# Optimization experiments

Hardware: AMD Instinct MI355X
Metric: run time of the kernel (lower is better)

## Reference

```python
import jax, jax.numpy as jnp
import numpy as np
from jax import lax

NUM_CLASSES = 10
NUM_ITER = 3
CAP_DIM = 8       # primary capsule dim
OUT_CAP_DIM = 16  # digit capsule dim
NUM_MAP = 32      # 256 / 8
NUM_PRIM = 144    # 12*12


def squash(x, axis=-1):
    s2 = jnp.sum(x * x, axis=axis, keepdims=True)
    return (s2 / (1.0 + s2)) * x / jnp.sqrt(s2 + 1e-8)


def conv2d(x, w, b):
    y = lax.conv_general_dilated(x, w, (1, 1), 'VALID',
                                 dimension_numbers=('NCHW', 'OIHW', 'NCHW'))
    return y + b[None, :, None, None]


def setup_inputs() -> dict:
    key = jax.random.key(0)
    ks = jax.random.split(key, 13)
    B = 128
    return {
        'imgs': jax.random.uniform(ks[0], (B, 1, 28, 28), dtype=jnp.float32),
        'conv1_w': jax.random.normal(ks[1], (256, 1, 9, 9), jnp.float32) * 0.05,
        'conv1_b': jnp.zeros((256,), jnp.float32),
        'conv2_w': jax.random.normal(ks[2], (256, 256, 9, 9), jnp.float32) * 0.02,
        'conv2_b': jnp.zeros((256,), jnp.float32),
        # non-shared routing weights: [num_prim_map, num_prim_cap, num_classes, out_dim, in_dim]
        'W_digit': jax.random.normal(ks[3], (NUM_MAP, NUM_PRIM, NUM_CLASSES, OUT_CAP_DIM, CAP_DIM), jnp.float32),
        'dec_w1': jax.random.normal(ks[4], (OUT_CAP_DIM * NUM_CLASSES, 512), jnp.float32) * 0.05,
        'dec_b1': jnp.zeros((512,), jnp.float32),
        'dec_w2': jax.random.normal(ks[5], (512, 1024), jnp.float32) * 0.04,
        'dec_b2': jnp.zeros((1024,), jnp.float32),
        'dec_w3': jax.random.normal(ks[6], (1024, 784), jnp.float32) * 0.03,
        'dec_b3': jnp.zeros((784,), jnp.float32),
    }


def capsnet_fwd(imgs, conv1_w, conv1_b, conv2_w, conv2_b, W_digit,
                dec_w1, dec_b1, dec_w2, dec_b2, dec_w3, dec_b3):
    B = imgs.shape[0]
    # conv1 + relu: [B,256,20,20]
    x = jax.nn.relu(conv2d(imgs, conv1_w, conv1_b))
    # primary caps conv: [B,256,12,12]
    p = conv2d(x, conv2_w, conv2_b)
    # view [B, cap_dim, num_map, 12, 12] -> [B, num_map, 144, cap_dim]
    p = p.reshape(B, CAP_DIM, NUM_MAP, NUM_PRIM)
    p = jnp.transpose(p, (0, 2, 3, 1))
    u = squash(p, axis=-1)  # [B, 32, 144, 8]

    # u_hat[b,m,p,c,o] = W[m,p,c,o,i] * u[b,m,p,i]  (broadcast instead of repeat)
    u_hat = jnp.einsum('mpcoi,bmpi->bmpco', W_digit, u)
    u_hat = u_hat.reshape(B, NUM_MAP * NUM_PRIM, NUM_CLASSES, OUT_CAP_DIM)  # [B,4608,10,16]

    # dynamic routing
    b_ij = jnp.zeros((B, NUM_MAP * NUM_PRIM, NUM_CLASSES), u_hat.dtype)
    v = None
    for i in range(NUM_ITER):
        c_ij = jax.nn.softmax(b_ij, axis=1)                     # over input capsules
        s_j = jnp.einsum('bnc,bncd->bcd', c_ij, u_hat)          # [B,10,16]
        v = squash(s_j, axis=-1)
        if i != NUM_ITER - 1:
            b_ij = b_ij + jnp.einsum('bncd,bcd->bnc', u_hat, v)  # agreement

    # v: [B,10,16]
    v_length = jnp.sqrt(jnp.sum(v * v, axis=-1))                 # [B,10]
    y_pred = jnp.argmax(v_length, axis=1)
    y_pred_ohe = jax.nn.one_hot(y_pred, NUM_CLASSES, dtype=jnp.int32)

    masked = (v * y_pred_ohe.astype(v.dtype)[:, :, None]).reshape(B, -1)  # [B,160]
    h = jax.nn.relu(masked @ dec_w1 + dec_b1)
    h = jax.nn.relu(h @ dec_w2 + dec_b2)
    img_reconst = jax.nn.sigmoid(h @ dec_w3 + dec_b3)            # [B,784]
    return y_pred_ohe, img_reconst, v_length


def reference(imgs, conv1_w, conv1_b, conv2_w, conv2_b, W_digit,
              dec_w1, dec_b1, dec_w2, dec_b2, dec_w3, dec_b3):
    return capsnet_fwd(imgs, conv1_w, conv1_b, conv2_w, conv2_b, W_digit,
                       dec_w1, dec_b1, dec_w2, dec_b2, dec_w3, dec_b3)
```

## Files before the change

kernel.cpp:

```cpp
#include <hip/hip_runtime.h>
#include <cstdint>
#include <cstddef>

#define BB 128
#define NMAP 32
#define NPRIM 144
#define NCAP 4608
#define NCLS 10
#define ODIM 16
#define IDIM 8

#define WS_X1H  0
#define WS_X1L  6553600
#define WS_BH   13107200
#define WS_P    18415616
#define WS_U    23134208
#define WS_V    27852800
#define WS_H1   27873280
#define WS_H2   27938816
#define WS_CLS  28069888

#define OUT_REC  1280
#define OUT_LEN  101632

typedef __attribute__((ext_vector_type(8))) short short8;
typedef __attribute__((ext_vector_type(4))) float f32x4;

static __device__ __forceinline__ ushort f2bf(float f) {
    uint u = __float_as_uint(f);
    u = (u + 0x7FFFu + ((u >> 16) & 1u)) >> 16;
    return (ushort)u;
}
static __device__ __forceinline__ float bf2f(ushort h) {
    return __uint_as_float(((uint)h) << 16);
}

static __device__ __forceinline__ void gload16(const ushort* g, ushort* l) {
    __builtin_amdgcn_global_load_lds(
        (const __attribute__((address_space(1))) void*)g,
        (__attribute__((address_space(3))) void*)l, 16, 0, 0);
}


__global__ __launch_bounds__(256) void k_conv1(const float* __restrict__ img,
                                               const float* __restrict__ w,
                                               const float* __restrict__ bias,
                                               ushort* __restrict__ x1h,
                                               ushort* __restrict__ x1l) {
    __shared__ float simg[252];
    int bi = blockIdx.x;
    int y = bi % 20;
    int b = bi / 20;
    int oc = threadIdx.x;
    if (threadIdx.x < 252)
        simg[threadIdx.x] = img[(size_t)b * 784 + y * 28 + threadIdx.x];
    __syncthreads();

    float acc[20];
    float bv = bias[oc];
#pragma unroll
    for (int x = 0; x < 20; ++x) acc[x] = bv;
    const float* wp = w + oc * 81;
#pragma unroll
    for (int kh = 0; kh < 9; ++kh) {
        float r[28];
#pragma unroll
        for (int j = 0; j < 28; ++j) r[j] = simg[kh * 28 + j];
#pragma unroll
        for (int kw = 0; kw < 9; ++kw) {
            float wv = wp[kh * 9 + kw];
#pragma unroll
            for (int x = 0; x < 20; ++x)
                acc[x] = fmaf(wv, r[x + kw], acc[x]);
        }
    }
    size_t base = ((size_t)b * 400 + y * 20) * 256 + oc;
#pragma unroll
    for (int x = 0; x < 20; ++x) {
        float v = fmaxf(acc[x], 0.f);
        ushort h = f2bf(v);
        ushort lo = f2bf(v - bf2f(h));
        x1h[base + (size_t)x * 256] = h;
        x1l[base + (size_t)x * 256] = lo;
    }
}

__global__ __launch_bounds__(256) void k_prep_w2(const float* __restrict__ w2,
                                                 ushort* __restrict__ bpk) {
    int blk = blockIdx.x;
    int icc = blk >> 5, kq = (blk >> 3) & 3, ocg = blk & 7;
    int tid = threadIdx.x;
    int ocl = tid >> 3, ic8 = tid & 7;
    int oc = ocg * 32 + ocl;
    int ic = icc * 32 + kq * 8 + ic8;
    const float* src = w2 + ((size_t)oc * 256 + ic) * 81;
    size_t dbase = (size_t)icc * 16384 + (size_t)kq * 2048 + (size_t)oc * 8 + ic8;
#pragma unroll 9
    for (int t = 0; t < 81; ++t) {
        float v = src[t];
        ushort h = f2bf(v);
        ushort lo = f2bf(v - bf2f(h));
        bpk[(size_t)t * 131072 + dbase] = h;
        bpk[(size_t)t * 131072 + dbase + 8192] = lo;
    }
}

static __device__ __forceinline__ f32x4 mfma16(short8 a, short8 b, f32x4 c) {
    return __builtin_amdgcn_mfma_f32_16x16x32_bf16(a, b, c, 0, 0, 0);
}


template<int NMF>
static __device__ __forceinline__ void tap_body(
    f32x4 (&acc)[5][2], const ushort* A_lds, const ushort* Bc,
    const int* celloff, int tapoff, int bro0, int bro1) {
    short8 ah[5], al[5];
#pragma unroll
    for (int i = 0; i < NMF; ++i) {
        ah[i] = *(const short8*)(A_lds + tapoff + celloff[i]);
        al[i] = *(const short8*)(A_lds + 16000 + tapoff + celloff[i]);
    }
    short8 bh0 = *(const short8*)(Bc + bro0);
    short8 bh1 = *(const short8*)(Bc + bro1);
    short8 bl0 = *(const short8*)(Bc + 4096 + bro0);
    short8 bl1 = *(const short8*)(Bc + 4096 + bro1);
#pragma unroll
    for (int i = 0; i < NMF; ++i) {
        acc[i][0] = mfma16(ah[i], bh0, acc[i][0]);
        acc[i][1] = mfma16(ah[i], bh1, acc[i][1]);
    }
#pragma unroll
    for (int i = 0; i < NMF; ++i) {
        acc[i][0] = mfma16(ah[i], bl0, acc[i][0]);
        acc[i][1] = mfma16(ah[i], bl1, acc[i][1]);
    }
#pragma unroll
    for (int i = 0; i < NMF; ++i) {
        acc[i][0] = mfma16(al[i], bh0, acc[i][0]);
        acc[i][1] = mfma16(al[i], bh1, acc[i][1]);
    }
}

template<int MF0, int NMF>
static __device__ __forceinline__ void conv2s_epi(
    const f32x4 (&acc)[5][2], const float* __restrict__ bias,
    float* __restrict__ p, int b, int oc0, int nq, int r, int kq) {
#pragma unroll
    for (int j = 0; j < 2; ++j) {
        int oc = oc0 + (nq * 2 + j) * 16 + r;
        float bv = bias[oc];
#pragma unroll
        for (int i = 0; i < NMF; ++i) {
            int row = b * 144 + (MF0 + i) * 16 + kq * 4;
#pragma unroll
            for (int reg = 0; reg < 4; ++reg)
                p[(size_t)(row + reg) * 256 + oc] = acc[i][j][reg] + bv;
        }
    }
}

__global__ __launch_bounds__(512, 2) void k_conv2s(
    const ushort* __restrict__ x1h, const ushort* __restrict__ x1l,
    const ushort* __restrict__ bpk,
    const float* __restrict__ bias, float* __restrict__ p) {
    __shared__ __align__(16) ushort A_lds[32000];
    __shared__ __align__(16) ushort Bb[16384];

    const int tid = threadIdx.x;
    const int lane = tid & 63;
    const int wv = tid >> 6;
    const int mh = wv >> 2;
    const int nq = wv & 3;
    const int b  = blockIdx.x >> 1;
    const int nt = blockIdx.x & 1;
    const int oc0 = nt * 128;
    const int r = lane & 15, kq = lane >> 4;
    const int MF0r = mh ? 5 : 0;

    int celloff[5];
#pragma unroll
    for (int i = 0; i < 5; ++i) {
        int lm = (MF0r + i) * 16 + r;
        celloff[i] = ((lm / 12) * 20 + (lm % 12)) * 40 + kq * 8;
    }
    const int bro0 = kq * 1024 + ((nq * 2 + 0) * 16 + r) * 8;
    const int bro1 = kq * 1024 + ((nq * 2 + 1) * 16 + r) * 8;

    const int comp_w = wv >> 2, kq_w = wv & 3;
    const ushort* gB0 = bpk + comp_w * 8192 + kq_w * 2048 + oc0 * 8 + lane * 8;
    ushort* lB0 = Bb + comp_w * 4096 + kq_w * 1024;

    f32x4 acc[5][2];
#pragma unroll
    for (int i = 0; i < 5; ++i)
#pragma unroll
        for (int j = 0; j < 2; ++j)
            acc[i][j] = (f32x4){0.f, 0.f, 0.f, 0.f};

    for (int icc = 0; icc < 8; ++icc) {
#pragma unroll
        for (int rd = 0; rd < 7; ++rd) {
            int idx = rd * 512 + tid;
            if (idx < 3200) {
                int comp = (idx >= 1600) ? 1 : 0;
                int ci = idx - comp * 1600;
                int cell = ci >> 2, cc = ci & 3;
                const ushort* src = (comp ? x1l : x1h) +
                    ((size_t)b * 400 + cell) * 256 + icc * 32 + cc * 8;
                short8 val = *(const short8*)src;
                *(short8*)(A_lds + comp * 16000 + cell * 40 + cc * 8) = val;
            }
        }
        {
            size_t goff = (size_t)icc * 16384;
            gload16(gB0 + goff, lB0);
            gload16(gB0 + goff + 512, lB0 + 512);
        }
        __syncthreads();

#pragma unroll 2
        for (int t = 0; t < 81; ++t) {
            const int cur = t & 1;
            if (t < 80) {
                size_t goff = (size_t)(t + 1) * 131072 + (size_t)icc * 16384;
                gload16(gB0 + goff, lB0 + (cur ^ 1) * 8192);
                gload16(gB0 + goff + 512, lB0 + (cur ^ 1) * 8192 + 512);
            }
            int kh = t / 9, kw = t - kh * 9;
            int tapoff = (kh * 20 + kw) * 40;
            const ushort* Bc = Bb + cur * 8192;
            if (mh == 0) tap_body<5>(acc, A_lds, Bc, celloff, tapoff, bro0, bro1);
            else         tap_body<4>(acc, A_lds, Bc, celloff, tapoff, bro0, bro1);
            __syncthreads();
        }
    }

    if (mh == 0) conv2s_epi<0, 5>(acc, bias, p, b, oc0, nq, r, kq);
    else         conv2s_epi<5, 4>(acc, bias, p, b, oc0, nq, r, kq);
}

__global__ __launch_bounds__(256) void k_squash(const float* __restrict__ p,
                                                float* __restrict__ u) {
    int id = blockIdx.x * 256 + threadIdx.x;
    int n = id % NCAP;
    int b = id / NCAP;
    int m = n / NPRIM, pos = n - m * NPRIM;
    const float* pp = p + ((size_t)b * 144 + pos) * 256 + m;
    float pv[8];
    float s2 = 0.f;
#pragma unroll
    for (int i = 0; i < 8; ++i) {
        pv[i] = pp[i * 32];
        s2 = fmaf(pv[i], pv[i], s2);
    }
    float f = (s2 / (1.f + s2)) / sqrtf(s2 + 1e-8f);
    float4 a = make_float4(f * pv[0], f * pv[1], f * pv[2], f * pv[3]);
    float4 c = make_float4(f * pv[4], f * pv[5], f * pv[6], f * pv[7]);
    float4* up = (float4*)(u + (size_t)id * 8);
    up[0] = a;
    up[1] = c;
}

__global__ __launch_bounds__(256) void k_prep_wt(const float* __restrict__ Wd,
                                                 float* __restrict__ Wt) {
    __shared__ float S[64][129];
    int c = blockIdx.x % NCLS;
    int nt = blockIdx.x / NCLS;
    int n0 = nt * 64;
    int tid = threadIdx.x;
#pragma unroll
    for (int rep = 0; rep < 32; ++rep) {
        int idx = rep * 256 + tid;
        int nl = idx >> 7, oi = idx & 127;
        S[nl][oi] = Wd[(size_t)(n0 + nl) * 1280 + c * 128 + oi];
    }
    __syncthreads();
#pragma unroll
    for (int rep = 0; rep < 32; ++rep) {
        int idx = rep * 256 + tid;
        int oi = idx >> 6, nl = idx & 63;
        Wt[((size_t)c * 128 + oi) * NCAP + n0 + nl] = S[nl][oi];
    }
}

__global__ __launch_bounds__(256) void k_route5(const float* __restrict__ u,
                                                const float* __restrict__ Wt,
                                                float* __restrict__ v_out) {
    __shared__ float part[4][2][17];
    __shared__ float sums[2][17];
    __shared__ float vsh[2][16];
    int c = blockIdx.x % NCLS;
    int bg = blockIdx.x / NCLS;
    int b0 = bg * 2;
    int tid = threadIdx.x;
    int lane = tid & 63, wvi = tid >> 6;
    const float* WtC = Wt + (size_t)c * 128 * NCAP;

    float bij[18][2];
#pragma unroll
    for (int j = 0; j < 18; ++j) { bij[j][0] = 0.f; bij[j][1] = 0.f; }

    for (int iter = 0; iter < 3; ++iter) {
        float sZ[2] = {0.f, 0.f};
        float sS[2][16];
#pragma unroll
        for (int o = 0; o < 16; ++o) { sS[0][o] = 0.f; sS[1][o] = 0.f; }

        for (int j = 0; j < 18; ++j) {
            int n = j * 256 + tid;
            const float4* up0 = (const float4*)(u + ((size_t)b0 * NCAP + n) * 8);
            const float4* up1 = (const float4*)(u + ((size_t)(b0 + 1) * NCAP + n) * 8);
            float4 a0 = up0[0], a1 = up0[1];
            float4 c0 = up1[0], c1 = up1[1];
            float u0[8] = {a0.x, a0.y, a0.z, a0.w, a1.x, a1.y, a1.z, a1.w};
            float u1[8] = {c0.x, c0.y, c0.z, c0.w, c1.x, c1.y, c1.z, c1.w};
            float uh[2][16];
#pragma unroll
            for (int o = 0; o < 16; ++o) {
                float s0 = 0.f, s1 = 0.f;
#pragma unroll
                for (int i = 0; i < 8; ++i) {
                    float w = WtC[(size_t)(o * 8 + i) * NCAP + n];
                    s0 = fmaf(w, u0[i], s0);
                    s1 = fmaf(w, u1[i], s1);
                }
                uh[0][o] = s0;
                uh[1][o] = s1;
            }
#pragma unroll
            for (int bb = 0; bb < 2; ++bb) {
                float e;
                if (iter == 0) {
                    e = 1.f;
                } else {
                    float agr = 0.f;
#pragma unroll
                    for (int o = 0; o < 16; ++o) agr = fmaf(uh[bb][o], vsh[bb][o], agr);
                    bij[j][bb] += agr;
                    e = __expf(bij[j][bb]);
                }
                sZ[bb] += e;
#pragma unroll
                for (int o = 0; o < 16; ++o) sS[bb][o] = fmaf(e, uh[bb][o], sS[bb][o]);
            }
        }

#pragma unroll
        for (int bb = 0; bb < 2; ++bb) {
            float z = sZ[bb];
#pragma unroll
            for (int d = 32; d >= 1; d >>= 1) z += __shfl_xor(z, d, 64);
            if (lane == 0) part[wvi][bb][0] = z;
#pragma unroll
            for (int o = 0; o < 16; ++o) {
                float s = sS[bb][o];
#pragma unroll
                for (int d = 32; d >= 1; d >>= 1) s += __shfl_xor(s, d, 64);
                if (lane == 0) part[wvi][bb][1 + o] = s;
            }
        }
        __syncthreads();
        if (tid < 34) {
            int bb = tid / 17, k = tid % 17;
            float s = 0.f;
#pragma unroll
            for (int w4 = 0; w4 < 4; ++w4) s += part[w4][bb][k];
            sums[bb][k] = s;
        }
        __syncthreads();
        if (tid < 2) {
            float Z = sums[tid][0];
            float s[16];
            float s2 = 0.f;
#pragma unroll
            for (int o = 0; o < 16; ++o) {
                s[o] = sums[tid][1 + o] / Z;
                s2 = fmaf(s[o], s[o], s2);
            }
            float f = (s2 / (1.f + s2)) / sqrtf(s2 + 1e-8f);
#pragma unroll
            for (int o = 0; o < 16; ++o) vsh[tid][o] = f * s[o];
        }
        __syncthreads();
    }
    if (tid < 32) {
        int bb = tid >> 4, o = tid & 15;
        v_out[((size_t)(b0 + bb) * NCLS + c) * 16 + o] = vsh[bb][o];
    }
}

__global__ __launch_bounds__(64) void k_head(const float* __restrict__ v,
                                             float* __restrict__ out,
                                             int* __restrict__ cls_ws) {
    __shared__ float len2[NCLS];
    __shared__ int cls_sh;
    int b = blockIdx.x, tid = threadIdx.x;
    if (tid < NCLS) {
        float s2 = 0.f;
#pragma unroll
        for (int o = 0; o < 16; ++o) {
            float t = v[((size_t)b * NCLS + tid) * 16 + o];
            s2 = fmaf(t, t, s2);
        }
        len2[tid] = s2;
        out[OUT_LEN + b * NCLS + tid] = sqrtf(s2);
    }
    __syncthreads();
    if (tid == 0) {
        int best = 0;
        float bv = len2[0];
        for (int c2 = 1; c2 < NCLS; ++c2)
            if (len2[c2] > bv) { bv = len2[c2]; best = c2; }
        cls_sh = best;
        cls_ws[b] = best;
    }
    __syncthreads();
    if (tid < NCLS) out[b * NCLS + tid] = (tid == cls_sh) ? 1.0f : 0.0f;
}

__global__ __launch_bounds__(256) void k_dec1(const float* __restrict__ v,
                                              const int* __restrict__ cls_ws,
                                              const float* __restrict__ w1,
                                              const float* __restrict__ b1,
                                              float* __restrict__ h1) {
    int id = blockIdx.x * 256 + threadIdx.x;
    int j = id % 512, b = id / 512;
    int cls = cls_ws[b];
    const float* vp = v + ((size_t)b * NCLS + cls) * 16;
    float acc = b1[j];
#pragma unroll
    for (int o = 0; o < 16; ++o)
        acc = fmaf(vp[o], w1[(size_t)(cls * 16 + o) * 512 + j], acc);
    h1[id] = fmaxf(acc, 0.f);
}

__global__ __launch_bounds__(256) void k_dec2(const float* __restrict__ h1,
                                              const float* __restrict__ w2,
                                              const float* __restrict__ b2,
                                              float* __restrict__ h2) {
    __shared__ float hs[512];
    int bi = blockIdx.x;
    int jc = bi % 4;
    int b = bi / 4;
    int tid = threadIdx.x;
    hs[tid] = h1[b * 512 + tid];
    hs[tid + 256] = h1[b * 512 + tid + 256];
    __syncthreads();
    int j = jc * 256 + tid;
    float acc = b2[j];
#pragma unroll 8
    for (int k = 0; k < 512; ++k)
        acc = fmaf(hs[k], w2[(size_t)k * 1024 + j], acc);
    h2[b * 1024 + j] = fmaxf(acc, 0.f);
}

__global__ __launch_bounds__(256) void k_dec3(const float* __restrict__ h2,
                                              const float* __restrict__ w3,
                                              const float* __restrict__ b3,
                                              float* __restrict__ out) {
    __shared__ float hs[1024];
    int bi = blockIdx.x;
    int jc = bi % 4;
    int b = bi / 4;
    int tid = threadIdx.x;
#pragma unroll
    for (int t = 0; t < 4; ++t) hs[tid + t * 256] = h2[b * 1024 + tid + t * 256];
    __syncthreads();
    int j = jc * 256 + tid;
    if (j < 784) {
        float acc = b3[j];
#pragma unroll 8
        for (int k = 0; k < 1024; ++k)
            acc = fmaf(hs[k], w3[(size_t)k * 784 + j], acc);
        out[OUT_REC + b * 784 + j] = 1.f / (1.f + __expf(-acc));
    }
}

extern "C" void kernel_launch(void* const* d_in, const int* in_sizes, int n_in,
                              void* d_out, int out_size, void* d_ws, size_t ws_size,
                              hipStream_t stream) {
    const float* imgs = (const float*)d_in[0];
    const float* c1w  = (const float*)d_in[1];
    const float* c1b  = (const float*)d_in[2];
    const float* c2w  = (const float*)d_in[3];
    const float* c2b  = (const float*)d_in[4];
    const float* Wd   = (const float*)d_in[5];
    const float* dw1  = (const float*)d_in[6];
    const float* db1  = (const float*)d_in[7];
    const float* dw2  = (const float*)d_in[8];
    const float* db2  = (const float*)d_in[9];
    const float* dw3  = (const float*)d_in[10];
    const float* db3  = (const float*)d_in[11];

    float* out = (float*)d_out;
    float* ws  = (float*)d_ws;
    ushort* x1h = (ushort*)(ws + WS_X1H);
    ushort* x1l = (ushort*)(ws + WS_X1L);
    ushort* bpk = (ushort*)(ws + WS_BH);
    float* p    = ws + WS_P;
    float* u    = ws + WS_U;
    float* v    = ws + WS_V;
    float* h1   = ws + WS_H1;
    float* h2   = ws + WS_H2;
    int*   cls  = (int*)(ws + WS_CLS);
    float* wt32 = ws + WS_X1H;

    k_conv1<<<BB * 20, 256, 0, stream>>>(imgs, c1w, c1b, x1h, x1l);
    k_prep_w2<<<256, 256, 0, stream>>>(c2w, bpk);
    k_conv2s<<<BB * 2, 512, 0, stream>>>(x1h, x1l, bpk, c2b, p);
    k_squash<<<BB * NCAP / 256, 256, 0, stream>>>(p, u);
    k_prep_wt<<<720, 256, 0, stream>>>(Wd, wt32);
    k_route5<<<(BB / 2) * NCLS, 256, 0, stream>>>(u, wt32, v);
    k_head<<<BB, 64, 0, stream>>>(v, out, cls);
    k_dec1<<<BB * 512 / 256, 256, 0, stream>>>(v, cls, dw1, db1, h1);
    k_dec2<<<BB * 4, 256, 0, stream>>>(h1, dw2, db2, h2);
    k_dec3<<<BB * 4, 256, 0, stream>>>(h2, dw3, db3, out);
}
```

Baseline: 1.299 ms.

## Deepen conv2 B-tile pipeline to six LDS stages with register double-buffered fragments

The primary-caps conv kernel now uses a six-slot LDS ring for the per-tap weight tiles, prefetching four taps ahead instead of one. It processes two taps per barrier and preloads the A/B fragments for the next pair into registers while the current pair's MFMAs run. This halves the number of __syncthreads and hides LDS and global latency behind matrix work. In exchange it uses more LDS (Bb grows to 96KB) and many more registers for the two fragment sets. The launch bound is changed to a waves-per-eu attribute, which could cost occupancy or cause spills.

```diff
diff --git a/kernel.cpp b/kernel.cpp
--- a/kernel.cpp
+++ b/kernel.cpp
@@ -110,34 +110,52 @@
 }
 
 
+struct FragR { short8 ah[5], al[5], bh0, bh1, bl0, bl1; };
+
 template<int NMF>
-static __device__ __forceinline__ void tap_body(
-    f32x4 (&acc)[5][2], const ushort* A_lds, const ushort* Bc,
-    const int* celloff, int tapoff, int bro0, int bro1) {
-    short8 ah[5], al[5];
+static __device__ __forceinline__ void pre_fragR(
+    FragR& f, const ushort* A_lds, const ushort* Bb, int tn,
+    const int* celloff, int bro0, int bro1) {
+    int kh = tn / 9, kw = tn - kh * 9;
+    int tapoff = (kh * 20 + kw) * 40;
+    const ushort* Bc = Bb + (tn % 6) * 8192;
 #pragma unroll
     for (int i = 0; i < NMF; ++i) {
-        ah[i] = *(const short8*)(A_lds + tapoff + celloff[i]);
-        al[i] = *(const short8*)(A_lds + 16000 + tapoff + celloff[i]);
-    }
-    short8 bh0 = *(const short8*)(Bc + bro0);
-    short8 bh1 = *(const short8*)(Bc + bro1);
-    short8 bl0 = *(const short8*)(Bc + 4096 + bro0);
-    short8 bl1 = *(const short8*)(Bc + 4096 + bro1);
+        f.ah[i] = *(const short8*)(A_lds + tapoff + celloff[i]);
+        f.al[i] = *(const short8*)(A_lds + 16000 + tapoff + celloff[i]);
+    }
+    f.bh0 = *(const short8*)(Bc + bro0);
+    f.bh1 = *(const short8*)(Bc + bro1);
+    f.bl0 = *(const short8*)(Bc + 4096 + bro0);
+    f.bl1 = *(const short8*)(Bc + 4096 + bro1);
+}
+
+template<int NMF>
+static __device__ __forceinline__ void mfma_fragR(f32x4 (&acc)[5][2], const FragR& f) {
 #pragma unroll
     for (int i = 0; i < NMF; ++i) {
-        acc[i][0] = mfma16(ah[i], bh0, acc[i][0]);
-        acc[i][1] = mfma16(ah[i], bh1, acc[i][1]);
+        acc[i][0] = mfma16(f.ah[i], f.bh0, acc[i][0]);
+        acc[i][1] = mfma16(f.ah[i], f.bh1, acc[i][1]);
     }
 #pragma unroll
     for (int i = 0; i < NMF; ++i) {
-        acc[i][0] = mfma16(ah[i], bl0, acc[i][0]);
-        acc[i][1] = mfma16(ah[i], bl1, acc[i][1]);
+        acc[i][0] = mfma16(f.ah[i], f.bl0, acc[i][0]);
+        acc[i][1] = mfma16(f.ah[i], f.bl1, acc[i][1]);
     }
 #pragma unroll
     for (int i = 0; i < NMF; ++i) {
-        acc[i][0] = mfma16(al[i], bh0, acc[i][0]);
-        acc[i][1] = mfma16(al[i], bh1, acc[i][1]);
+        acc[i][0] = mfma16(f.al[i], f.bh0, acc[i][0]);
+        acc[i][1] = mfma16(f.al[i], f.bh1, acc[i][1]);
+    }
+}
+
+static __device__ __forceinline__ void stage_tap(
+    const ushort* gB0, ushort* lB0, int tn, size_t gicc) {
+    if (tn <= 80) {
+        size_t g = (size_t)tn * 131072 + gicc;
+        ushort* d = lB0 + (tn % 6) * 8192;
+        gload16(gB0 + g, d);
+        gload16(gB0 + g + 512, d + 512);
     }
 }
 
@@ -159,12 +177,14 @@
     }
 }
 
-__global__ __launch_bounds__(512, 2) void k_conv2s(
+__global__ __launch_bounds__(512)
+__attribute__((amdgpu_waves_per_eu(2, 2)))
+void k_conv2s(
     const ushort* __restrict__ x1h, const ushort* __restrict__ x1l,
     const ushort* __restrict__ bpk,
     const float* __restrict__ bias, float* __restrict__ p) {
     __shared__ __align__(16) ushort A_lds[32000];
-    __shared__ __align__(16) ushort Bb[16384];
+    __shared__ __align__(16) ushort Bb[49152];
 
     const int tid = threadIdx.x;
     const int lane = tid & 63;
@@ -197,7 +217,10 @@
         for (int j = 0; j < 2; ++j)
             acc[i][j] = (f32x4){0.f, 0.f, 0.f, 0.f};
 
+    FragR fX, fY;
+
     for (int icc = 0; icc < 8; ++icc) {
+        const size_t gicc = (size_t)icc * 16384;
 #pragma unroll
         for (int rd = 0; rd < 7; ++rd) {
             int idx = rd * 512 + tid;
@@ -211,28 +234,49 @@
                 *(short8*)(A_lds + comp * 16000 + cell * 40 + cc * 8) = val;
             }
         }
-        {
-            size_t goff = (size_t)icc * 16384;
-            gload16(gB0 + goff, lB0);
-            gload16(gB0 + goff + 512, lB0 + 512);
-        }
+        stage_tap(gB0, lB0, 0, gicc);
+        stage_tap(gB0, lB0, 1, gicc);
+        stage_tap(gB0, lB0, 2, gicc);
+        stage_tap(gB0, lB0, 3, gicc);
         __syncthreads();
-
-#pragma unroll 2
-        for (int t = 0; t < 81; ++t) {
-            const int cur = t & 1;
-            if (t < 80) {
-                size_t goff = (size_t)(t + 1) * 131072 + (size_t)icc * 16384;
-                gload16(gB0 + goff, lB0 + (cur ^ 1) * 8192);
-                gload16(gB0 + goff + 512, lB0 + (cur ^ 1) * 8192 + 512);
+        if (mh == 0) {
+            pre_fragR<5>(fX, A_lds, Bb, 0, celloff, bro0, bro1);
+            pre_fragR<5>(fY, A_lds, Bb, 1, celloff, bro0, bro1);
+        } else {
+            pre_fragR<4>(fX, A_lds, Bb, 0, celloff, bro0, bro1);
+            pre_fragR<4>(fY, A_lds, Bb, 1, celloff, bro0, bro1);
+        }
+
+#pragma unroll 1
+        for (int ph = 0; ph < 39; ++ph) {
+            const int T = ph * 2;
+            stage_tap(gB0, lB0, T + 4, gicc);
+            stage_tap(gB0, lB0, T + 5, gicc);
+            if (mh == 0) {
+                mfma_fragR<5>(acc, fX);
+                mfma_fragR<5>(acc, fY);
+                pre_fragR<5>(fX, A_lds, Bb, T + 2, celloff, bro0, bro1);
+                pre_fragR<5>(fY, A_lds, Bb, T + 3, celloff, bro0, bro1);
+            } else {
+                mfma_fragR<4>(acc, fX);
+                mfma_fragR<4>(acc, fY);
+                pre_fragR<4>(fX, A_lds, Bb, T + 2, celloff, bro0, bro1);
+                pre_fragR<4>(fY, A_lds, Bb, T + 3, celloff, bro0, bro1);
             }
-            int kh = t / 9, kw = t - kh * 9;
-            int tapoff = (kh * 20 + kw) * 40;
-            const ushort* Bc = Bb + cur * 8192;
-            if (mh == 0) tap_body<5>(acc, A_lds, Bc, celloff, tapoff, bro0, bro1);
-            else         tap_body<4>(acc, A_lds, Bc, celloff, tapoff, bro0, bro1);
             __syncthreads();
         }
+        if (mh == 0) {
+            mfma_fragR<5>(acc, fX);
+            mfma_fragR<5>(acc, fY);
+            pre_fragR<5>(fX, A_lds, Bb, 80, celloff, bro0, bro1);
+            mfma_fragR<5>(acc, fX);
+        } else {
+            mfma_fragR<4>(acc, fX);
+            mfma_fragR<4>(acc, fY);
+            pre_fragR<4>(fX, A_lds, Bb, 80, celloff, bro0, bro1);
+            mfma_fragR<4>(acc, fX);
+        }
+        __syncthreads();
     }
 
     if (mh == 0) conv2s_epi<0, 5>(acc, bias, p, b, oc0, nq, r, kq);
```

Result: faster. 1.155 ms (-11.1%).
